# Optimization experiments

Hardware: AMD Instinct MI355X
Metric: run time of the kernel (lower is better)

The kernel has to match this reference:

```python
import jax, jax.numpy as jnp
import numpy as np

K = 3          # kernel_size
STRIDE = 1
PAD = 1
DIL = 1


def conv2d(x, w, b, stride=STRIDE, pad=PAD, dil=DIL):
    y = jax.lax.conv_general_dilated(
        x, w, window_strides=(stride, stride),
        padding=((pad, pad), (pad, pad)), rhs_dilation=(dil, dil),
        dimension_numbers=('NCHW', 'OIHW', 'NCHW'))
    if b is not None:
        y = y + b[None, :, None, None]
    return y


def bilinear_gather(x, py, px):
    """Zero-padded bilinear sampling.
    x: [B,C,H,W]; py,px: [B,K2,Ho,Wo] float coords. Returns [B,C,K2,Ho,Wo].
    Matches torchvision deform_conv2d: out-of-range corners contribute zero."""
    B, C, H, W = x.shape
    y0 = jnp.floor(py)
    x0 = jnp.floor(px)
    wy1 = py - y0
    wx1 = px - x0
    wy0 = 1.0 - wy1
    wx0 = 1.0 - wx1
    xf = x.reshape(B, C, H * W)

    def corner(yi, xi, wgt):
        valid = (yi >= 0) & (yi < H) & (xi >= 0) & (xi < W)
        yc = jnp.clip(yi, 0, H - 1).astype(jnp.int32)
        xc = jnp.clip(xi, 0, W - 1).astype(jnp.int32)
        idx = (yc * W + xc).reshape(B, 1, -1)            # [B,1,K2*Ho*Wo]
        v = jnp.take_along_axis(xf, idx, axis=2)         # [B,C,K2*Ho*Wo]
        v = v.reshape(B, C, *yi.shape[1:])               # [B,C,K2,Ho,Wo]
        w = (wgt * valid.astype(x.dtype))[:, None]       # [B,1,K2,Ho,Wo]
        return v * w

    return (corner(y0, x0, wy0 * wx0) + corner(y0, x0 + 1, wy0 * wx1)
            + corner(y0 + 1, x0, wy1 * wx0) + corner(y0 + 1, x0 + 1, wy1 * wx1))


def reference(x, w_offset, b_offset, w_mask, b_mask, w_deform):
    B, C, H, W = x.shape
    K2 = K * K
    offset = conv2d(x, w_offset, b_offset)               # [B,2*K2,Ho,Wo]
    mask = jax.nn.sigmoid(conv2d(x, w_mask, b_mask))     # [B,K2,Ho,Wo]
    Ho, Wo = offset.shape[2], offset.shape[3]

    off = offset.reshape(B, K2, 2, Ho, Wo)
    dy, dx = off[:, :, 0], off[:, :, 1]                  # [B,K2,Ho,Wo]

    ky = (jnp.arange(K2) // K).astype(x.dtype) * DIL     # kernel tap row offsets
    kx = (jnp.arange(K2) % K).astype(x.dtype) * DIL
    base_y = (jnp.arange(Ho) * STRIDE - PAD).astype(x.dtype)
    base_x = (jnp.arange(Wo) * STRIDE - PAD).astype(x.dtype)
    py = dy + base_y[None, None, :, None] + ky[None, :, None, None]
    px = dx + base_x[None, None, None, :] + kx[None, :, None, None]

    val = bilinear_gather(x, py, px)                     # [B,C,K2,Ho,Wo]
    val = val * mask[:, None]                            # modulation

    w = w_deform.reshape(w_deform.shape[0], C, K2)       # [Cout,Cin,K2]
    return jnp.einsum('bckhw,ock->bohw', val, w)


def setup_inputs() -> dict:
    key = jax.random.key(0)
    k = jax.random.split(key, 6)
    B, Cin, Cout, H, W = 2, 64, 64, 224, 224
    x = jax.random.normal(k[0], (B, Cin, H, W), dtype=jnp.float32)
    # source zero-inits offset/mask convs; use small random weights to exercise
    # fractional, scattered sampling coordinates.
    w_offset = jax.random.normal(k[1], (2 * K * K, Cin, K, K), dtype=jnp.float32) * 0.01
    b_offset = jnp.zeros((2 * K * K,), dtype=jnp.float32)
    w_mask = jax.random.normal(k[2], (K * K, Cin, K, K), dtype=jnp.float32) * 0.01
    b_mask = jnp.zeros((K * K,), dtype=jnp.float32)
    w_deform = jax.random.normal(k[3], (Cout, Cin, K, K), dtype=jnp.float32) * (1.0 / np.sqrt(Cin * K * K))
    return {"x": x, "w_offset": w_offset, "b_offset": b_offset,
            "w_mask": w_mask, "b_mask": b_mask, "w_deform": w_deform}
```

## Files before the change

### kernel.cpp

```cpp
#include <hip/hip_runtime.h>
#include <hip/hip_bf16.h>
#include <math.h>

constexpr int B    = 2;
constexpr int C    = 64;
constexpr int H    = 224;
constexpr int W    = 224;
constexpr int Hp   = 226;
constexpr int Wp   = 226;
constexpr int K2   = 9;
constexpr int OCO  = 18;
constexpr int OM   = 27;
constexpr int COUT = 64;
constexpr int HW   = H * W;
constexpr int NPIX = B * HW;
constexpr int CK   = C * K2;

typedef short  bf16x8 __attribute__((ext_vector_type(8)));
typedef float  f32x4  __attribute__((ext_vector_type(4)));

__device__ inline unsigned short f2bf(float f) {
    union { float f; unsigned u; } v; v.f = f;
    unsigned r = v.u + 0x7FFF + ((v.u >> 16) & 1);
    return (unsigned short)(r >> 16);
}
__device__ inline unsigned cvtpk(float a, float b) {
    __hip_bfloat162 h = __float22bfloat162_rn(make_float2(a, b));
    union { __hip_bfloat162 h; unsigned u; } cv; cv.h = h;
    return cv.u;
}

__global__ __launch_bounds__(256) void k_padT(const float* __restrict__ x,
                                              float* __restrict__ xp) {
    __shared__ float tile[32][33];
    const int b   = blockIdx.z;
    const int hw0 = blockIdx.x * 32;
    const int c0  = blockIdx.y * 32;
    const int tx  = threadIdx.x;
    const int ty  = threadIdx.y;
    const float* xb  = x  + (size_t)b * C * HW;
    float*       xpb = xp + (size_t)b * Hp * Wp * C;
#pragma unroll
    for (int j = 0; j < 4; ++j) {
        int c = c0 + ty + j * 8;
        tile[ty + j * 8][tx] = xb[(size_t)c * HW + hw0 + tx];
    }
    __syncthreads();
#pragma unroll
    for (int j = 0; j < 4; ++j) {
        int hw = hw0 + ty + j * 8;
        int y  = hw / W;
        int xx = hw % W;
        xpb[((size_t)(y + 1) * Wp + (xx + 1)) * C + c0 + tx] = tile[tx][ty + j * 8];
    }
}

__global__ void k_border(float* __restrict__ xp) {
    int i = blockIdx.x * 256 + threadIdx.x;
    if (i >= B * 900 * 16) return;
    int chunk = i & 15;
    int cell  = (i >> 4) % 900;
    int b     = (i >> 4) / 900;
    int y, x;
    if      (cell < 226) { y = 0;              x = cell; }
    else if (cell < 452) { y = Hp - 1;         x = cell - 226; }
    else if (cell < 676) { y = cell - 452 + 1; x = 0; }
    else                 { y = cell - 676 + 1; x = Wp - 1; }
    float4 z = make_float4(0.f, 0.f, 0.f, 0.f);
    *reinterpret_cast<float4*>(xp + ((size_t)b * Hp * Wp + y * Wp + x) * C + chunk * 4) = z;
}

__global__ void k_wA(const float* __restrict__ wd, unsigned short* __restrict__ wA) {
    int i = blockIdx.x * 256 + threadIdx.x;
    if (i >= COUT * CK) return;
    int o  = i / CK;
    int kc = i % CK;
    int k  = kc >> 6;
    int c  = kc & 63;
    wA[i] = f2bf(wd[((size_t)o * C + c) * 9 + k]);
}

__global__ void k_womA(const float* __restrict__ w_off,
                       const float* __restrict__ w_msk,
                       const float* __restrict__ b_off,
                       const float* __restrict__ b_msk,
                       unsigned short* __restrict__ womA,
                       float* __restrict__ biasv) {
    int i = blockIdx.x * 256 + threadIdx.x;
    if (i < 32) biasv[i] = (i < OCO) ? b_off[i] : (i < OM) ? b_msk[i - OCO] : 0.f;
    if (i >= 32 * CK) return;
    int oc = i / CK;
    int kc = i % CK;
    int k  = kc >> 6;
    int c  = kc & 63;
    float v = (oc < OCO) ? w_off[((size_t)oc * C + c) * 9 + k]
            : (oc < OM)  ? w_msk[((size_t)(oc - OCO) * C + c) * 9 + k]
                         : 0.f;
    womA[i] = f2bf(v);
}

__global__ __launch_bounds__(256) void k_convom(const float* __restrict__ xp,
                                                const unsigned short* __restrict__ womA,
                                                const float* __restrict__ biasv,
                                                int4* __restrict__ gtabO,
                                                float4* __restrict__ gtabW) {
    __shared__ __align__(16) unsigned short imcol[64 * CK];
    const int tid  = threadIdx.x;
    const int lane = tid & 63;
    const int wv   = tid >> 6;
    const int q    = lane >> 4;
    const int l15  = lane & 15;
    const int pix0 = blockIdx.x * 64;
    const int bb   = pix0 / HW;
    const float* xb = xp + (size_t)bb * Hp * Wp * C;

    const int c0 = l15 * 4;
    for (int pi = 0; pi < 4; ++pi) {
        const int p_local = wv * 16 + pi * 4 + q;
        const int pix = pix0 + p_local;
        const int hw  = pix - bb * HW;
        const int y   = hw / W;
        const int xx  = hw % W;
        int wbase = p_local * (CK * 2) + l15 * 8;
        wbase ^= (p_local & 7) << 4;
#pragma unroll
        for (int k = 0; k < 9; ++k) {
            const int ky = k / 3, kx = k % 3;
            const float4 v = *reinterpret_cast<const float4*>(
                xb + ((size_t)(y + ky) * Wp + (xx + kx)) * C + c0);
            *reinterpret_cast<uint2*>(reinterpret_cast<char*>(imcol) + wbase + k * 128) =
                make_uint2(cvtpk(v.x, v.y), cvtpk(v.z, v.w));
        }
    }
    __syncthreads();

    f32x4 acc0 = {0.f, 0.f, 0.f, 0.f}, acc1 = {0.f, 0.f, 0.f, 0.f};
    const unsigned short* a0 = womA + (size_t)l15 * CK;
    const unsigned short* a1 = womA + (size_t)(16 + l15) * CK;
    const int row = wv * 16 + l15;
#pragma unroll 3
    for (int ks = 0; ks < 18; ++ks) {
        int byte = row * (CK * 2) + ks * 64 + q * 16;
        byte ^= (row & 7) << 4;
        const bf16x8 bfv = *reinterpret_cast<const bf16x8*>(
            reinterpret_cast<const char*>(imcol) + byte);
        const bf16x8 af0 = *reinterpret_cast<const bf16x8*>(a0 + ks * 32 + q * 8);
        const bf16x8 af1 = *reinterpret_cast<const bf16x8*>(a1 + ks * 32 + q * 8);
        acc0 = __builtin_amdgcn_mfma_f32_16x16x32_bf16(af0, bfv, acc0, 0, 0, 0);
        acc1 = __builtin_amdgcn_mfma_f32_16x16x32_bf16(af1, bfv, acc1, 0, 0, 0);
    }

    __syncthreads();
    float* som = reinterpret_cast<float*>(imcol);
    {
        const int p = wv * 16 + l15;
#pragma unroll
        for (int r = 0; r < 4; ++r) {
            const int oc = q * 4 + r;
            som[p * 28 + oc] = acc0[r] + biasv[oc];
        }
#pragma unroll
        for (int r = 0; r < 4; ++r) {
            const int oc = 16 + q * 4 + r;
            if (oc < OM) {
                float v = acc1[r] + biasv[oc];
                som[p * 28 + oc] = (oc < OCO) ? v : 1.0f / (1.0f + __expf(-v));
            }
        }
    }
    __syncthreads();

    for (int e = tid; e < 64 * 9; e += 256) {
        const int p  = e / 9;
        const int k  = e - p * 9;
        const int pix = pix0 + p;
        const int hw  = pix - bb * HW;
        const int ho  = hw / W;
        const int wo  = hw - ho * W;
        const int ky  = k / 3, kx = k - (k / 3) * 3;
        const float dy = som[p * 28 + 2 * k];
        const float dx = som[p * 28 + 2 * k + 1];
        const float m  = som[p * 28 + OCO + k];
        const float py = dy + (float)(ho + ky - 1);
        const float px = dx + (float)(wo + kx - 1);
        const float fy = floorf(py), fx = floorf(px);
        const int   y0 = (int)fy,   x0 = (int)fx;
        const float wy1 = py - fy,  wx1 = px - fx;
        const float wy0 = 1.f - wy1, wx0 = 1.f - wx1;
        const bool iy0 = (y0 >= 0) & (y0 < H);
        const bool iy1 = (y0 + 1 >= 0) & (y0 + 1 < H);
        const bool ix0 = (x0 >= 0) & (x0 < W);
        const bool ix1 = (x0 + 1 >= 0) & (x0 + 1 < W);
        const int ya = min(max(y0 + 1, 0), Hp - 1);
        const int yb = min(max(y0 + 2, 0), Hp - 1);
        const int xa = min(max(x0 + 1, 0), Wp - 1);
        const int xc = min(max(x0 + 2, 0), Wp - 1);
        const int rA = ya * Wp, rB = yb * Wp;
        gtabO[(size_t)pix * 9 + k] = make_int4((rA + xa) * C, (rA + xc) * C,
                                               (rB + xa) * C, (rB + xc) * C);
        gtabW[(size_t)pix * 9 + k] = make_float4(
            wy0 * wx0 * m * ((iy0 & ix0) ? 1.f : 0.f),
            wy0 * wx1 * m * ((iy0 & ix1) ? 1.f : 0.f),
            wy1 * wx0 * m * ((iy1 & ix0) ? 1.f : 0.f),
            wy1 * wx1 * m * ((iy1 & ix1) ? 1.f : 0.f));
    }
}

constexpr int PPB = 64;

__global__ __launch_bounds__(256) void k_deform(const float* __restrict__ xp,
                                                const int4* __restrict__ gtabO,
                                                const float4* __restrict__ gtabW,
                                                const unsigned short* __restrict__ wA,
                                                float* __restrict__ out) {
    __shared__ __align__(16) unsigned short valT[64 * CK];
    const int tid  = threadIdx.x;
    const int lane = tid & 63;
    const int wv   = tid >> 6;
    const int q    = lane >> 4;
    const int l15  = lane & 15;
    const int pix0 = blockIdx.x * PPB;
    const int bb   = pix0 / HW;
    const float* xb = xp + (size_t)bb * Hp * Wp * C;

    const int c0 = l15 * 4;
    for (int pi = 0; pi < 4; ++pi) {
        const int p_local = wv * 16 + pi * 4 + q;
        const int pix = pix0 + p_local;
        const int4*   gO = gtabO + (size_t)pix * 9;
        const float4* gW = gtabW + (size_t)pix * 9;
        int wbase = p_local * (CK * 2) + l15 * 8;
        wbase ^= (p_local & 7) << 4;
#pragma unroll
        for (int k = 0; k < 9; ++k) {
            const int4   o  = gO[k];
            const float4 wt = gW[k];
            const float4 v00 = *reinterpret_cast<const float4*>(xb + o.x + c0);
            const float4 v01 = *reinterpret_cast<const float4*>(xb + o.y + c0);
            const float4 v10 = *reinterpret_cast<const float4*>(xb + o.z + c0);
            const float4 v11 = *reinterpret_cast<const float4*>(xb + o.w + c0);
            const float s0 = wt.x * v00.x + wt.y * v01.x + wt.z * v10.x + wt.w * v11.x;
            const float s1 = wt.x * v00.y + wt.y * v01.y + wt.z * v10.y + wt.w * v11.y;
            const float s2 = wt.x * v00.z + wt.y * v01.z + wt.z * v10.z + wt.w * v11.z;
            const float s3 = wt.x * v00.w + wt.y * v01.w + wt.z * v10.w + wt.w * v11.w;
            *reinterpret_cast<uint2*>(reinterpret_cast<char*>(valT) + wbase + k * 128) =
                make_uint2(cvtpk(s0, s1), cvtpk(s2, s3));
        }
    }
    __syncthreads();

    f32x4 acc[4] = {{0.f,0.f,0.f,0.f},{0.f,0.f,0.f,0.f},{0.f,0.f,0.f,0.f},{0.f,0.f,0.f,0.f}};
    const unsigned short* wrow = wA + (size_t)(wv * 16 + l15) * CK;
#pragma unroll 3
    for (int ks = 0; ks < 18; ++ks) {
        const bf16x8 af = *reinterpret_cast<const bf16x8*>(wrow + ks * 32 + q * 8);
#pragma unroll
        for (int nt = 0; nt < 4; ++nt) {
            const int row = nt * 16 + l15;
            int byte = row * (CK * 2) + ks * 64 + q * 16;
            byte ^= (row & 7) << 4;
            const bf16x8 bfv = *reinterpret_cast<const bf16x8*>(
                reinterpret_cast<const char*>(valT) + byte);
            acc[nt] = __builtin_amdgcn_mfma_f32_16x16x32_bf16(af, bfv, acc[nt], 0, 0, 0);
        }
    }

    const int o0 = wv * 16 + q * 4;
#pragma unroll
    for (int nt = 0; nt < 4; ++nt) {
        const int pixn = pix0 + nt * 16 + l15;
        const int hw   = pixn - bb * HW;
#pragma unroll
        for (int r = 0; r < 4; ++r)
            out[((size_t)bb * COUT + o0 + r) * HW + hw] = acc[nt][r];
    }
}

extern "C" void kernel_launch(void* const* d_in, const int* in_sizes, int n_in,
                              void* d_out, int out_size, void* d_ws, size_t ws_size,
                              hipStream_t stream) {
    const float* x     = (const float*)d_in[0];
    const float* w_off = (const float*)d_in[1];
    const float* b_off = (const float*)d_in[2];
    const float* w_msk = (const float*)d_in[3];
    const float* b_msk = (const float*)d_in[4];
    const float* w_def = (const float*)d_in[5];
    float* out = (float*)d_out;

    float* ws    = (float*)d_ws;
    float* xpadT = ws;
    int4*   gtabO = (int4*)(xpadT + (size_t)B * Hp * Wp * C);
    float4* gtabW = (float4*)(gtabO + (size_t)NPIX * 9);
    float*  biasv = (float*)(gtabW + (size_t)NPIX * 9);
    unsigned short* wA   = (unsigned short*)(biasv + 32);
    unsigned short* womA = wA + (size_t)COUT * CK;

    k_border<<<(B * 900 * 16 + 255) / 256, 256, 0, stream>>>(xpadT);
    k_padT<<<dim3(HW / 32, C / 32, B), dim3(32, 8), 0, stream>>>(x, xpadT);
    k_wA<<<(COUT * CK + 255) / 256, 256, 0, stream>>>(w_def, wA);
    k_womA<<<(32 * CK + 255) / 256, 256, 0, stream>>>(w_off, w_msk, b_off, b_msk,
                                                      womA, biasv);
    k_convom<<<NPIX / 64, 256, 0, stream>>>(xpadT, womA, biasv, gtabO, gtabW);
    k_deform<<<NPIX / PPB, 256, 0, stream>>>(xpadT, gtabO, gtabW, wA, out);
}
```

Measured before the change: 204.4 us.

## Store padded input as bf16 and shrink blocks to 32 pixels with XCD swizzle

The padded channel-last copy of x is now written in bf16. The offset/mask conv copies it directly into shared memory, and the deform gather reads half the bytes per corner before unpacking to fp32. Both main kernels now process 32 pixels per block with a blockIdx remap across 8 groups and a 4-blocks-per-CU launch bound, which shrinks LDS use to raise occupancy. In exchange, bilinear sampling sees bf16-rounded inputs, and weight fragments are reloaded more often per output pixel.

```diff
diff --git a/kernel.cpp b/kernel.cpp
--- a/kernel.cpp
+++ b/kernel.cpp
@@ -15,6 +15,7 @@
 constexpr int HW   = H * W;
 constexpr int NPIX = B * HW;
 constexpr int CK   = C * K2;
+constexpr int CPB  = 32;
 
 typedef short  bf16x8 __attribute__((ext_vector_type(8)));
 typedef float  f32x4  __attribute__((ext_vector_type(4)));
@@ -29,45 +30,57 @@
     union { __hip_bfloat162 h; unsigned u; } cv; cv.h = h;
     return cv.u;
 }
+__device__ inline float blo(unsigned u) { union { unsigned u; float f; } c; c.u = u << 16; return c.f; }
+__device__ inline float bhi(unsigned u) { union { unsigned u; float f; } c; c.u = u & 0xFFFF0000u; return c.f; }
 
 __global__ __launch_bounds__(256) void k_padT(const float* __restrict__ x,
-                                              float* __restrict__ xp) {
-    __shared__ float tile[32][33];
-    const int b   = blockIdx.z;
+                                              unsigned short* __restrict__ xp) {
+    __shared__ float tile[64][33];
+    const int b   = blockIdx.y;
     const int hw0 = blockIdx.x * 32;
-    const int c0  = blockIdx.y * 32;
-    const int tx  = threadIdx.x;
-    const int ty  = threadIdx.y;
-    const float* xb  = x  + (size_t)b * C * HW;
-    float*       xpb = xp + (size_t)b * Hp * Wp * C;
-#pragma unroll
-    for (int j = 0; j < 4; ++j) {
-        int c = c0 + ty + j * 8;
-        tile[ty + j * 8][tx] = xb[(size_t)c * HW + hw0 + tx];
+    const int tid = threadIdx.x;
+    const int hwl = tid & 31, cl = tid >> 5;
+    const float* xb = x + (size_t)b * C * HW;
+#pragma unroll
+    for (int j = 0; j < 8; ++j) {
+        int c = cl + j * 8;
+        tile[c][hwl] = xb[(size_t)c * HW + hw0 + hwl];
     }
     __syncthreads();
-#pragma unroll
-    for (int j = 0; j < 4; ++j) {
-        int hw = hw0 + ty + j * 8;
-        int y  = hw / W;
-        int xx = hw % W;
-        xpb[((size_t)(y + 1) * Wp + (xx + 1)) * C + c0 + tx] = tile[tx][ty + j * 8];
-    }
-}
-
-__global__ void k_border(float* __restrict__ xp) {
+    unsigned short* xpb = xp + (size_t)b * Hp * Wp * C;
+    const int l15 = tid & 15, hh = tid >> 4;
+    const int c = l15 * 4;
+    {
+        int hw = hw0 + hh;
+        int y = hw / W, xx = hw % W;
+        float t0 = tile[c][hh], t1 = tile[c + 1][hh];
+        float t2 = tile[c + 2][hh], t3 = tile[c + 3][hh];
+        *reinterpret_cast<uint2*>(xpb + ((size_t)(y + 1) * Wp + (xx + 1)) * C + c) =
+            make_uint2(cvtpk(t0, t1), cvtpk(t2, t3));
+    }
+    {
+        int hw = hw0 + 16 + hh;
+        int y = hw / W, xx = hw % W;
+        float t0 = tile[c][16 + hh], t1 = tile[c + 1][16 + hh];
+        float t2 = tile[c + 2][16 + hh], t3 = tile[c + 3][16 + hh];
+        *reinterpret_cast<uint2*>(xpb + ((size_t)(y + 1) * Wp + (xx + 1)) * C + c) =
+            make_uint2(cvtpk(t0, t1), cvtpk(t2, t3));
+    }
+}
+
+__global__ void k_border(unsigned short* __restrict__ xp) {
     int i = blockIdx.x * 256 + threadIdx.x;
-    if (i >= B * 900 * 16) return;
-    int chunk = i & 15;
-    int cell  = (i >> 4) % 900;
-    int b     = (i >> 4) / 900;
+    if (i >= B * 900 * 8) return;
+    int chunk = i & 7;
+    int cell  = (i >> 3) % 900;
+    int b     = (i >> 3) / 900;
     int y, x;
     if      (cell < 226) { y = 0;              x = cell; }
     else if (cell < 452) { y = Hp - 1;         x = cell - 226; }
     else if (cell < 676) { y = cell - 452 + 1; x = 0; }
     else                 { y = cell - 676 + 1; x = Wp - 1; }
-    float4 z = make_float4(0.f, 0.f, 0.f, 0.f);
-    *reinterpret_cast<float4*>(xp + ((size_t)b * Hp * Wp + y * Wp + x) * C + chunk * 4) = z;
+    uint4 z = make_uint4(0u, 0u, 0u, 0u);
+    *reinterpret_cast<uint4*>(xp + ((size_t)b * Hp * Wp + y * Wp + x) * C + chunk * 8) = z;
 }
 
 __global__ void k_wA(const float* __restrict__ wd, unsigned short* __restrict__ wA) {
@@ -99,24 +112,28 @@
     womA[i] = f2bf(v);
 }
 
-__global__ __launch_bounds__(256) void k_convom(const float* __restrict__ xp,
-                                                const unsigned short* __restrict__ womA,
-                                                const float* __restrict__ biasv,
-                                                int4* __restrict__ gtabO,
-                                                float4* __restrict__ gtabW) {
-    __shared__ __align__(16) unsigned short imcol[64 * CK];
+__global__ __launch_bounds__(256, 4) void k_convom(const unsigned short* __restrict__ xp,
+                                                   const unsigned short* __restrict__ womA,
+                                                   const float* __restrict__ biasv,
+                                                   int4* __restrict__ gtabO,
+                                                   float4* __restrict__ gtabW) {
+    __shared__ __align__(16) unsigned short imcol[CPB * CK];
+    __shared__ float som[CPB][28];
     const int tid  = threadIdx.x;
     const int lane = tid & 63;
     const int wv   = tid >> 6;
     const int q    = lane >> 4;
     const int l15  = lane & 15;
-    const int pix0 = blockIdx.x * 64;
+    int bid = blockIdx.x;
+    bid = (bid & 7) * (gridDim.x >> 3) + (bid >> 3);
+    const int pix0 = bid * CPB;
     const int bb   = pix0 / HW;
-    const float* xb = xp + (size_t)bb * Hp * Wp * C;
+    const unsigned short* xb = xp + (size_t)bb * Hp * Wp * C;
 
     const int c0 = l15 * 4;
-    for (int pi = 0; pi < 4; ++pi) {
-        const int p_local = wv * 16 + pi * 4 + q;
+#pragma unroll
+    for (int pi = 0; pi < 2; ++pi) {
+        const int p_local = pi * 16 + wv * 4 + q;
         const int pix = pix0 + p_local;
         const int hw  = pix - bb * HW;
         const int y   = hw / W;
@@ -126,51 +143,41 @@
 #pragma unroll
         for (int k = 0; k < 9; ++k) {
             const int ky = k / 3, kx = k % 3;
-            const float4 v = *reinterpret_cast<const float4*>(
+            const uint2 v = *reinterpret_cast<const uint2*>(
                 xb + ((size_t)(y + ky) * Wp + (xx + kx)) * C + c0);
-            *reinterpret_cast<uint2*>(reinterpret_cast<char*>(imcol) + wbase + k * 128) =
-                make_uint2(cvtpk(v.x, v.y), cvtpk(v.z, v.w));
+            *reinterpret_cast<uint2*>(reinterpret_cast<char*>(imcol) + wbase + k * 128) = v;
         }
     }
     __syncthreads();
 
-    f32x4 acc0 = {0.f, 0.f, 0.f, 0.f}, acc1 = {0.f, 0.f, 0.f, 0.f};
-    const unsigned short* a0 = womA + (size_t)l15 * CK;
-    const unsigned short* a1 = womA + (size_t)(16 + l15) * CK;
-    const int row = wv * 16 + l15;
+    f32x4 acc = {0.f, 0.f, 0.f, 0.f};
+    const int m = wv & 1, n = wv >> 1;
+    const unsigned short* a0 = womA + (size_t)(m * 16 + l15) * CK;
+    const int row = n * 16 + l15;
 #pragma unroll 3
     for (int ks = 0; ks < 18; ++ks) {
         int byte = row * (CK * 2) + ks * 64 + q * 16;
         byte ^= (row & 7) << 4;
         const bf16x8 bfv = *reinterpret_cast<const bf16x8*>(
             reinterpret_cast<const char*>(imcol) + byte);
-        const bf16x8 af0 = *reinterpret_cast<const bf16x8*>(a0 + ks * 32 + q * 8);
-        const bf16x8 af1 = *reinterpret_cast<const bf16x8*>(a1 + ks * 32 + q * 8);
-        acc0 = __builtin_amdgcn_mfma_f32_16x16x32_bf16(af0, bfv, acc0, 0, 0, 0);
-        acc1 = __builtin_amdgcn_mfma_f32_16x16x32_bf16(af1, bfv, acc1, 0, 0, 0);
-    }
-
-    __syncthreads();
-    float* som = reinterpret_cast<float*>(imcol);
+        const bf16x8 af = *reinterpret_cast<const bf16x8*>(a0 + ks * 32 + q * 8);
+        acc = __builtin_amdgcn_mfma_f32_16x16x32_bf16(af, bfv, acc, 0, 0, 0);
+    }
+
     {
-        const int p = wv * 16 + l15;
+        const int p = n * 16 + l15;
 #pragma unroll
         for (int r = 0; r < 4; ++r) {
-            const int oc = q * 4 + r;
-            som[p * 28 + oc] = acc0[r] + biasv[oc];
-        }
-#pragma unroll
-        for (int r = 0; r < 4; ++r) {
-            const int oc = 16 + q * 4 + r;
+            const int oc = m * 16 + q * 4 + r;
             if (oc < OM) {
-                float v = acc1[r] + biasv[oc];
-                som[p * 28 + oc] = (oc < OCO) ? v : 1.0f / (1.0f + __expf(-v));
+                float v = acc[r] + biasv[oc];
+                som[p][oc] = (oc < OCO) ? v : 1.0f / (1.0f + __expf(-v));
             }
         }
     }
     __syncthreads();
 
-    for (int e = tid; e < 64 * 9; e += 256) {
+    for (int e = tid; e < CPB * 9; e += 256) {
         const int p  = e / 9;
         const int k  = e - p * 9;
         const int pix = pix0 + p;
@@ -178,9 +185,9 @@
         const int ho  = hw / W;
         const int wo  = hw - ho * W;
         const int ky  = k / 3, kx = k - (k / 3) * 3;
-        const float dy = som[p * 28 + 2 * k];
-        const float dx = som[p * 28 + 2 * k + 1];
-        const float m  = som[p * 28 + OCO + k];
+        const float dy = som[p][2 * k];
+        const float dx = som[p][2 * k + 1];
+        const float mm = som[p][OCO + k];
         const float py = dy + (float)(ho + ky - 1);
         const float px = dx + (float)(wo + kx - 1);
         const float fy = floorf(py), fx = floorf(px);
@@ -199,33 +206,34 @@
         gtabO[(size_t)pix * 9 + k] = make_int4((rA + xa) * C, (rA + xc) * C,
                                                (rB + xa) * C, (rB + xc) * C);
         gtabW[(size_t)pix * 9 + k] = make_float4(
-            wy0 * wx0 * m * ((iy0 & ix0) ? 1.f : 0.f),
-            wy0 * wx1 * m * ((iy0 & ix1) ? 1.f : 0.f),
-            wy1 * wx0 * m * ((iy1 & ix0) ? 1.f : 0.f),
-            wy1 * wx1 * m * ((iy1 & ix1) ? 1.f : 0.f));
-    }
-}
-
-constexpr int PPB = 64;
-
-__global__ __launch_bounds__(256) void k_deform(const float* __restrict__ xp,
-                                                const int4* __restrict__ gtabO,
-                                                const float4* __restrict__ gtabW,
-                                                const unsigned short* __restrict__ wA,
-                                                float* __restrict__ out) {
-    __shared__ __align__(16) unsigned short valT[64 * CK];
+            wy0 * wx0 * mm * ((iy0 & ix0) ? 1.f : 0.f),
+            wy0 * wx1 * mm * ((iy0 & ix1) ? 1.f : 0.f),
+            wy1 * wx0 * mm * ((iy1 & ix0) ? 1.f : 0.f),
+            wy1 * wx1 * mm * ((iy1 & ix1) ? 1.f : 0.f));
+    }
+}
+
+__global__ __launch_bounds__(256, 4) void k_deform(const unsigned short* __restrict__ xp,
+                                                   const int4* __restrict__ gtabO,
+                                                   const float4* __restrict__ gtabW,
+                                                   const unsigned short* __restrict__ wA,
+                                                   float* __restrict__ out) {
+    __shared__ __align__(16) unsigned short valT[CPB * CK];
     const int tid  = threadIdx.x;
     const int lane = tid & 63;
     const int wv   = tid >> 6;
     const int q    = lane >> 4;
     const int l15  = lane & 15;
-    const int pix0 = blockIdx.x * PPB;
+    int bid = blockIdx.x;
+    bid = (bid & 7) * (gridDim.x >> 3) + (bid >> 3);
+    const int pix0 = bid * CPB;
     const int bb   = pix0 / HW;
-    const float* xb = xp + (size_t)bb * Hp * Wp * C;
+    const unsigned short* xb = xp + (size_t)bb * Hp * Wp * C;
 
     const int c0 = l15 * 4;
-    for (int pi = 0; pi < 4; ++pi) {
-        const int p_local = wv * 16 + pi * 4 + q;
+#pragma unroll
+    for (int pi = 0; pi < 2; ++pi) {
+        const int p_local = pi * 16 + wv * 4 + q;
         const int pix = pix0 + p_local;
         const int4*   gO = gtabO + (size_t)pix * 9;
         const float4* gW = gtabW + (size_t)pix * 9;
@@ -235,27 +243,27 @@
         for (int k = 0; k < 9; ++k) {
             const int4   o  = gO[k];
             const float4 wt = gW[k];
-            const float4 v00 = *reinterpret_cast<const float4*>(xb + o.x + c0);
-            const float4 v01 = *reinterpret_cast<const float4*>(xb + o.y + c0);
-            const float4 v10 = *reinterpret_cast<const float4*>(xb + o.z + c0);
-            const float4 v11 = *reinterpret_cast<const float4*>(xb + o.w + c0);
-            const float s0 = wt.x * v00.x + wt.y * v01.x + wt.z * v10.x + wt.w * v11.x;
-            const float s1 = wt.x * v00.y + wt.y * v01.y + wt.z * v10.y + wt.w * v11.y;
-            const float s2 = wt.x * v00.z + wt.y * v01.z + wt.z * v10.z + wt.w * v11.z;
-            const float s3 = wt.x * v00.w + wt.y * v01.w + wt.z * v10.w + wt.w * v11.w;
+            const uint2 u00 = *reinterpret_cast<const uint2*>(xb + o.x + c0);
+            const uint2 u01 = *reinterpret_cast<const uint2*>(xb + o.y + c0);
+            const uint2 u10 = *reinterpret_cast<const uint2*>(xb + o.z + c0);
+            const uint2 u11 = *reinterpret_cast<const uint2*>(xb + o.w + c0);
+            const float s0 = wt.x * blo(u00.x) + wt.y * blo(u01.x) + wt.z * blo(u10.x) + wt.w * blo(u11.x);
+            const float s1 = wt.x * bhi(u00.x) + wt.y * bhi(u01.x) + wt.z * bhi(u10.x) + wt.w * bhi(u11.x);
+            const float s2 = wt.x * blo(u00.y) + wt.y * blo(u01.y) + wt.z * blo(u10.y) + wt.w * blo(u11.y);
+            const float s3 = wt.x * bhi(u00.y) + wt.y * bhi(u01.y) + wt.z * bhi(u10.y) + wt.w * bhi(u11.y);
             *reinterpret_cast<uint2*>(reinterpret_cast<char*>(valT) + wbase + k * 128) =
                 make_uint2(cvtpk(s0, s1), cvtpk(s2, s3));
         }
     }
     __syncthreads();
 
-    f32x4 acc[4] = {{0.f,0.f,0.f,0.f},{0.f,0.f,0.f,0.f},{0.f,0.f,0.f,0.f},{0.f,0.f,0.f,0.f}};
+    f32x4 acc[2] = {{0.f,0.f,0.f,0.f},{0.f,0.f,0.f,0.f}};
     const unsigned short* wrow = wA + (size_t)(wv * 16 + l15) * CK;
 #pragma unroll 3
     for (int ks = 0; ks < 18; ++ks) {
         const bf16x8 af = *reinterpret_cast<const bf16x8*>(wrow + ks * 32 + q * 8);
 #pragma unroll
-        for (int nt = 0; nt < 4; ++nt) {
+        for (int nt = 0; nt < 2; ++nt) {
             const int row = nt * 16 + l15;
             int byte = row * (CK * 2) + ks * 64 + q * 16;
             byte ^= (row & 7) << 4;
@@ -267,7 +275,7 @@
 
     const int o0 = wv * 16 + q * 4;
 #pragma unroll
-    for (int nt = 0; nt < 4; ++nt) {
+    for (int nt = 0; nt < 2; ++nt) {
         const int pixn = pix0 + nt * 16 + l15;
         const int hw   = pixn - bb * HW;
 #pragma unroll
@@ -287,19 +295,18 @@
     const float* w_def = (const float*)d_in[5];
     float* out = (float*)d_out;
 
-    float* ws    = (float*)d_ws;
-    float* xpadT = ws;
+    unsigned short* xpadT = (unsigned short*)d_ws;
     int4*   gtabO = (int4*)(xpadT + (size_t)B * Hp * Wp * C);
     float4* gtabW = (float4*)(gtabO + (size_t)NPIX * 9);
     float*  biasv = (float*)(gtabW + (size_t)NPIX * 9);
     unsigned short* wA   = (unsigned short*)(biasv + 32);
     unsigned short* womA = wA + (size_t)COUT * CK;
 
-    k_border<<<(B * 900 * 16 + 255) / 256, 256, 0, stream>>>(xpadT);
-    k_padT<<<dim3(HW / 32, C / 32, B), dim3(32, 8), 0, stream>>>(x, xpadT);
+    k_border<<<(B * 900 * 8 + 255) / 256, 256, 0, stream>>>(xpadT);
+    k_padT<<<dim3(HW / 32, B), 256, 0, stream>>>(x, xpadT);
     k_wA<<<(COUT * CK + 255) / 256, 256, 0, stream>>>(w_def, wA);
     k_womA<<<(32 * CK + 255) / 256, 256, 0, stream>>>(w_off, w_msk, b_off, b_msk,
                                                       womA, biasv);
-    k_convom<<<NPIX / 64, 256, 0, stream>>>(xpadT, womA, biasv, gtabO, gtabW);
-    k_deform<<<NPIX / PPB, 256, 0, stream>>>(xpadT, gtabO, gtabW, wA, out);
-}
+    k_convom<<<NPIX / CPB, 256, 0, stream>>>(xpadT, womA, biasv, gtabO, gtabW);
+    k_deform<<<NPIX / CPB, 256, 0, stream>>>(xpadT, gtabO, gtabW, wA, out);
+}
```

New measurement: 200.7 us. No clear change (-1.8%).
